# Kernel optimization log

Hardware: AMD Instinct MI355X
Metric: run time of the kernel (lower is better)

The kernel has to match this reference:

```python
import jax, jax.numpy as jnp
import numpy as np

B, C, H_IMG, W_IMG = 16, 384, 56, 56
NUM_HEADS = 6
HEAD_DIM = C // NUM_HEADS
BN_EPS = 1e-5


def _bn(x, gamma, beta, mean, var):
    # x: [b, ch, n] or [b, ch, h, w]; per-channel affine normalization (eval-mode BatchNorm)
    shape = (1, -1) + (1,) * (x.ndim - 2)
    scale = (gamma / jnp.sqrt(var + BN_EPS)).reshape(shape)
    shift = (beta - mean * gamma / jnp.sqrt(var + BN_EPS)).reshape(shape)
    return x * scale + shift


def setup_inputs() -> dict:
    key = jax.random.key(0)
    ks = jax.random.split(key, 12)
    c2 = 2 * C
    return {
        "x": jax.random.normal(ks[0], (B, C, H_IMG, W_IMG), jnp.float32),
        "qk_w": jax.random.normal(ks[1], (c2, C // 2), jnp.float32) * 0.05,
        "qk_gamma": jax.random.uniform(ks[2], (c2,), jnp.float32, 0.5, 1.5),
        "qk_beta": jax.random.normal(ks[3], (c2,), jnp.float32) * 0.1,
        "qk_mean": jax.random.normal(ks[4], (c2,), jnp.float32) * 0.1,
        "qk_var": jax.random.uniform(ks[5], (c2,), jnp.float32, 0.5, 1.5),
        "pe_w": jax.random.normal(ks[6], (C, 1, 3, 3), jnp.float32) * 0.1,
        "pe_gamma": jax.random.uniform(ks[7], (C,), jnp.float32, 0.5, 1.5),
        "pe_beta": jax.random.normal(ks[8], (C,), jnp.float32) * 0.1,
        "pe_mean": jax.random.normal(ks[9], (C,), jnp.float32) * 0.1,
        "pe_var": jax.random.uniform(ks[10], (C,), jnp.float32, 0.5, 1.5),
    }


def reference(x, qk_w, qk_gamma, qk_beta, qk_mean, qk_var,
              pe_w, pe_gamma, pe_beta, pe_mean, pe_var):
    b, c, h, w = x.shape
    n = h * w
    s = n ** (-0.5)
    nh, hd = NUM_HEADS, HEAD_DIM

    # grouped (groups=2) 1x1 conv: out channels [0:c] from input [0:c/2], [c:2c] from [c/2:c]
    xg = x.reshape(b, 2, c // 2, n)                       # [b, 2, c/2, n]
    wg = qk_w.reshape(2, c, c // 2)                       # [group, out_per_group, in_per_group]
    qk = jnp.einsum('bgin,goi->bgon', xg, wg).reshape(b, 2 * c, n)
    qk = _bn(qk, qk_gamma, qk_beta, qk_mean, qk_var)
    qk = jax.nn.elu(qk) + 1.0

    qk = qk.reshape(b, 2, nh, hd, n)
    q, k = qk[:, 0], qk[:, 1]                             # [b, H, d, n]
    v = x.reshape(b, nh, hd, n)                           # [b, H, d, n]

    # kv = (k*s) @ (v^T * s): [b, H, d, d]
    kv = jnp.einsum('bhdn,bhen->bhde', k * s, v * s)
    # numerator: q^T @ kv -> [b, H, n, d]
    num = jnp.einsum('bhdn,bhde->bhne', q, kv)
    # denominator: q^T @ mean_n(k) -> [b, H, n]
    den = jnp.einsum('bhdn,bhd->bhn', q, k.mean(axis=-1)) + 1e-6
    attn = (num / den[..., None]).transpose(0, 1, 3, 2).reshape(b, c, h, w)

    # depthwise 3x3 conv positional encoding on v (= x) + BN
    pe = jax.lax.conv_general_dilated(
        x, pe_w, window_strides=(1, 1), padding=((1, 1), (1, 1)),
        feature_group_count=c, dimension_numbers=('NCHW', 'OIHW', 'NCHW'))
    pe = _bn(pe, pe_gamma, pe_beta, pe_mean, pe_var)

    return attn + pe
```

## Files before the change

### kernel.cpp

```cpp
#include <hip/hip_runtime.h>
#include <math.h>

#define N_SP 3136
#define BN_EPS 1e-5f

typedef __attribute__((ext_vector_type(8))) short short8;
typedef __attribute__((ext_vector_type(4))) float f32x4;

#define K_SZ    (16*384*N_SP)
#define QF_OFF  (K_SZ)
#define QF_FSZ  (16*6*49*8192/2)
#define KVP_OFF (QF_OFF + QF_FSZ)
#define KVP_SZ  (16*6*7*64*80)
#define KVT_OFF (KVP_OFF + KVP_SZ)
#define KVT_FSZ (2*96*80*64/2)
#define WH_OFF  (KVT_OFF + KVT_FSZ)
#define WSPLIT_N (2*384*192)

__device__ __forceinline__ void bsplit(float f, ushort& h, ushort& l) {
    uint u = __float_as_uint(f);
    uint hr = (u + 0x7FFFu + ((u >> 16) & 1u)) >> 16;
    h = (ushort)hr;
    float fh = __uint_as_float(hr << 16);
    float fl = f - fh;
    uint v = __float_as_uint(fl);
    l = (ushort)((v + 0x7FFFu + ((v >> 16) & 1u)) >> 16);
}

__global__ __launch_bounds__(256) void p0_wsplit(
    const float* __restrict__ qk_w, ushort* __restrict__ wh, ushort* __restrict__ wl)
{
    int idx = blockIdx.x * 256 + threadIdx.x;
    if (idx >= WSPLIT_N) return;
    ushort h, l;
    bsplit(qk_w[idx], h, l);
    wh[idx] = h;
    wl[idx] = l;
}

__global__ __launch_bounds__(256) void k1_qk_mfma(
    const float* __restrict__ x, const ushort* __restrict__ wh, const ushort* __restrict__ wl,
    const float* __restrict__ gamma, const float* __restrict__ beta,
    const float* __restrict__ mean, const float* __restrict__ var,
    float* __restrict__ k_out, ushort* __restrict__ qf)
{
    __shared__ __align__(16) ushort Ah[8192];
    __shared__ __align__(16) ushort Al[8192];
    __shared__ __align__(16) ushort Bh[4096];
    __shared__ __align__(16) ushort Bl[4096];

    const int bx = blockIdx.x;
    const int bz = blockIdx.y;
    const int by = blockIdx.z;
    const int b = bz >> 1, gg = bz & 1;
    const int t = threadIdx.x;
    const int lane = t & 63, wv = t >> 6;
    const int wr = wv >> 1, wc = wv & 1;
    const int lg = lane >> 4, l15 = lane & 15;

    f32x4 acc[4][2];
    #pragma unroll
    for (int m = 0; m < 4; ++m)
        #pragma unroll
        for (int nf = 0; nf < 2; ++nf)
            acc[m][nf] = (f32x4){0.f, 0.f, 0.f, 0.f};

    const float* xg = x + (size_t)(b * 384 + gg * 192) * N_SP + bx * 64;
    const ushort* whg = wh + (gg * 384 + by * 128) * 192;
    const ushort* wlg = wl + (gg * 384 + by * 128) * 192;

    for (int kt = 0; kt < 3; ++kt) {
        #pragma unroll
        for (int li = 0; li < 4; ++li) {
            int c = li * 256 + t;
            int row = c >> 3, kb = c & 7;
            int goff = row * 192 + kt * 64 + kb * 8;
            float4 vh = *(const float4*)(whg + goff);
            float4 vl = *(const float4*)(wlg + goff);
            int ch = (row * 8 + (kb ^ (row & 7))) * 8;
            *(float4*)&Ah[ch] = vh;
            *(float4*)&Al[ch] = vl;
        }
        #pragma unroll
        for (int li = 0; li < 2; ++li) {
            int idx = li * 256 + t;
            int kp = idx >> 4;
            int nq = idx & 15;
            int k0 = kp * 2;
            const float* px = xg + (size_t)(kt * 64 + k0) * N_SP + nq * 4;
            float4 v0 = *(const float4*)px;
            float4 v1 = *(const float4*)(px + N_SP);
            ushort h0[4], l0[4], h1[4], l1[4];
            float a0[4] = {v0.x, v0.y, v0.z, v0.w};
            float a1[4] = {v1.x, v1.y, v1.z, v1.w};
            #pragma unroll
            for (int i = 0; i < 4; ++i) { bsplit(a0[i], h0[i], l0[i]); bsplit(a1[i], h1[i], l1[i]); }
            int kb = k0 >> 3, ks = (k0 & 6) >> 1;
            #pragma unroll
            for (int i = 0; i < 4; ++i) {
                int n = nq * 4 + i;
                int chunk = n * 8 + (kb ^ ((n >> 1) & 7));
                ((uint*)Bh)[chunk * 4 + ks] = (uint)h0[i] | ((uint)h1[i] << 16);
                ((uint*)Bl)[chunk * 4 + ks] = (uint)l0[i] | ((uint)l1[i] << 16);
            }
        }
        __syncthreads();
        #pragma unroll
        for (int s = 0; s < 2; ++s) {
            short8 ah[4], al[4], bh[2], bl[2];
            int kb = s * 4 + lg;
            #pragma unroll
            for (int m = 0; m < 4; ++m) {
                int row = wr * 64 + m * 16 + l15;
                int ch = (row * 8 + (kb ^ (row & 7))) * 8;
                ah[m] = *(const short8*)&Ah[ch];
                al[m] = *(const short8*)&Al[ch];
            }
            #pragma unroll
            for (int nf = 0; nf < 2; ++nf) {
                int n = wc * 32 + nf * 16 + l15;
                int ch = (n * 8 + (kb ^ ((n >> 1) & 7))) * 8;
                bh[nf] = *(const short8*)&Bh[ch];
                bl[nf] = *(const short8*)&Bl[ch];
            }
            #pragma unroll
            for (int m = 0; m < 4; ++m)
                #pragma unroll
                for (int nf = 0; nf < 2; ++nf) {
                    acc[m][nf] = __builtin_amdgcn_mfma_f32_16x16x32_bf16(ah[m], bh[nf], acc[m][nf], 0, 0, 0);
                    acc[m][nf] = __builtin_amdgcn_mfma_f32_16x16x32_bf16(ah[m], bl[nf], acc[m][nf], 0, 0, 0);
                    acc[m][nf] = __builtin_amdgcn_mfma_f32_16x16x32_bf16(al[m], bh[nf], acc[m][nf], 0, 0, 0);
                }
        }
        __syncthreads();
    }

    float* scs = (float*)Bh;
    float* shs = scs + 128;
    if (t < 128) {
        int ch = gg * 384 + by * 128 + t;
        float sc = gamma[ch] / sqrtf(var[ch] + BN_EPS);
        scs[t] = sc;
        shs[t] = beta[ch] - mean[ch] * sc;
    }
    __syncthreads();

    if (gg == 0) {
        const int head = by * 2 + wr;
        ushort* qbase = qf + ((size_t)(b * 6 + head) * 49 + bx) * 8192;
        #pragma unroll
        for (int m = 0; m < 4; ++m) {
            #pragma unroll
            for (int nf = 0; nf < 2; ++nf) {
                ushort hh[4], ll[4];
                #pragma unroll
                for (int r = 0; r < 4; ++r) {
                    int orow = wr * 64 + m * 16 + lg * 4 + r;
                    float v = acc[m][nf][r] * scs[orow] + shs[orow];
                    v = v > 0.f ? v + 1.f : __expf(v);
                    bsplit(v, hh[r], ll[r]);
                }
                int hc = m * 4 + lg;
                int n = wc * 32 + nf * 16 + l15;
                uint2 uh, ul;
                uh.x = (uint)hh[0] | ((uint)hh[1] << 16);
                uh.y = (uint)hh[2] | ((uint)hh[3] << 16);
                ul.x = (uint)ll[0] | ((uint)ll[1] << 16);
                ul.y = (uint)ll[2] | ((uint)ll[3] << 16);
                *(uint2*)(qbase + (size_t)hc * 256 + n * 4) = uh;
                *(uint2*)(qbase + (size_t)(16 + hc) * 256 + n * 4) = ul;
            }
        }
    } else {
        size_t obase = ((size_t)b * 384 + by * 128) * N_SP + bx * 64 + wc * 32;
        #pragma unroll
        for (int m = 0; m < 4; ++m)
            #pragma unroll
            for (int nf = 0; nf < 2; ++nf) {
                #pragma unroll
                for (int r = 0; r < 4; ++r) {
                    int orow = wr * 64 + m * 16 + lg * 4 + r;
                    float v = acc[m][nf][r] * scs[orow] + shs[orow];
                    v = v > 0.f ? v + 1.f : __expf(v);
                    k_out[obase + (size_t)orow * N_SP + nf * 16 + l15] = v;
                }
            }
    }
}

__global__ __launch_bounds__(256) void k2_kv_mfma(
    const float* __restrict__ x, const float* __restrict__ kbuf,
    float* __restrict__ kv_part)
{
    __shared__ __align__(16) ushort Kh[4096], Kl[4096];
    __shared__ __align__(16) ushort Vh[5120], Vl[5120];

    const int chunk = blockIdx.x;
    const int h = blockIdx.y, b = blockIdx.z;
    const int t = threadIdx.x;
    const int lane = t & 63, wv = t >> 6;
    const int lg = lane >> 4, l15 = lane & 15;

    const float* kp = kbuf + (size_t)(b*384 + h*64) * N_SP;
    const float* vp = x   + (size_t)(b*384 + h*64) * N_SP;

    #pragma unroll
    for (int li = 0; li < 4; ++li) {
        int idx = li * 256 + t;
        int row = 64 + (idx >> 6), col = idx & 63;
        int off = (row * 8 + ((col >> 3) ^ (row & 7))) * 8 + (col & 7);
        Vh[off] = (row == 64) ? (ushort)0x3F80 : (ushort)0;
        Vl[off] = 0;
    }

    f32x4 acc[5];
    #pragma unroll
    for (int nf = 0; nf < 5; ++nf) acc[nf] = (f32x4){0.f, 0.f, 0.f, 0.f};

    for (int sub = 0; sub < 7; ++sub) {
        int n0 = chunk * 448 + sub * 64;
        #pragma unroll
        for (int li = 0; li < 4; ++li) {
            int idx = li * 256 + t;
            int row = idx >> 4, sc = idx & 15;
            int off = (row * 8 + ((sc >> 1) ^ (row & 7))) * 8 + (sc & 1) * 4;
            float4 kf = *(const float4*)&kp[(size_t)row * N_SP + n0 + sc * 4];
            ushort h0,h1,h2,h3,l0,l1,l2,l3;
            bsplit(kf.x,h0,l0); bsplit(kf.y,h1,l1); bsplit(kf.z,h2,l2); bsplit(kf.w,h3,l3);
            ((uint*)&Kh[off])[0] = (uint)h0 | ((uint)h1 << 16);
            ((uint*)&Kh[off])[1] = (uint)h2 | ((uint)h3 << 16);
            ((uint*)&Kl[off])[0] = (uint)l0 | ((uint)l1 << 16);
            ((uint*)&Kl[off])[1] = (uint)l2 | ((uint)l3 << 16);
            float4 vf = *(const float4*)&vp[(size_t)row * N_SP + n0 + sc * 4];
            bsplit(vf.x,h0,l0); bsplit(vf.y,h1,l1); bsplit(vf.z,h2,l2); bsplit(vf.w,h3,l3);
            ((uint*)&Vh[off])[0] = (uint)h0 | ((uint)h1 << 16);
            ((uint*)&Vh[off])[1] = (uint)h2 | ((uint)h3 << 16);
            ((uint*)&Vl[off])[0] = (uint)l0 | ((uint)l1 << 16);
            ((uint*)&Vl[off])[1] = (uint)l2 | ((uint)l3 << 16);
        }
        __syncthreads();
        #pragma unroll
        for (int s = 0; s < 2; ++s) {
            int arow = wv * 16 + l15;
            int akb = (s * 4 + lg) ^ (arow & 7);
            short8 ah = *(const short8*)&Kh[(arow * 8 + akb) * 8];
            short8 al = *(const short8*)&Kl[(arow * 8 + akb) * 8];
            #pragma unroll
            for (int nf = 0; nf < 5; ++nf) {
                int brow = nf * 16 + l15;
                int bkb = (s * 4 + lg) ^ (brow & 7);
                short8 bh = *(const short8*)&Vh[(brow * 8 + bkb) * 8];
                short8 bl = *(const short8*)&Vl[(brow * 8 + bkb) * 8];
                acc[nf] = __builtin_amdgcn_mfma_f32_16x16x32_bf16(ah, bh, acc[nf], 0, 0, 0);
                acc[nf] = __builtin_amdgcn_mfma_f32_16x16x32_bf16(ah, bl, acc[nf], 0, 0, 0);
                acc[nf] = __builtin_amdgcn_mfma_f32_16x16x32_bf16(al, bh, acc[nf], 0, 0, 0);
            }
        }
        __syncthreads();
    }

    size_t base = (size_t)((b*6 + h)*7 + chunk) * 64 * 80;
    #pragma unroll
    for (int nf = 0; nf < 5; ++nf)
        #pragma unroll
        for (int r = 0; r < 4; ++r) {
            int d = wv * 16 + lg * 4 + r;
            kv_part[base + (size_t)d * 80 + nf * 16 + l15] = acc[nf][r];
        }
}

__global__ __launch_bounds__(256) void k2b_reduce(
    const float* __restrict__ kv_part,
    ushort* __restrict__ kvt_h, ushort* __restrict__ kvt_l)
{
    const int bh = blockIdx.x;
    const int t = threadIdx.x;
    const float inv_n = 1.0f / (float)N_SP;
    const float* base = kv_part + (size_t)bh * 7 * 5120;
    ushort* oh = kvt_h + (size_t)bh * 5120;
    ushort* ol = kvt_l + (size_t)bh * 5120;
    float s[20];
    #pragma unroll
    for (int j = 0; j < 20; ++j) s[j] = 0.f;
    for (int c = 0; c < 7; ++c) {
        #pragma unroll
        for (int j = 0; j < 20; ++j) s[j] += base[c * 5120 + j * 256 + t];
    }
    #pragma unroll
    for (int j = 0; j < 20; ++j) {
        int i = j * 256 + t;
        int d = i / 80, e = i % 80;
        ushort h, l;
        bsplit(s[j] * inv_n, h, l);
        oh[e * 64 + d] = h;
        ol[e * 64 + d] = l;
    }
}

#define ATT_STRIDE 68
__global__ __launch_bounds__(256) void k3_attn_pe(
    const float* __restrict__ x, const ushort* __restrict__ qf,
    const ushort* __restrict__ kvt_h, const ushort* __restrict__ kvt_l,
    const float* __restrict__ pw,
    const float* __restrict__ pgamma, const float* __restrict__ pbeta,
    const float* __restrict__ pmean, const float* __restrict__ pvar,
    float* __restrict__ out)
{
    __shared__ __align__(16) float SBF[ATT_STRIDE * 64 + 64];

    const int bx = blockIdx.x;
    const int h = blockIdx.y, b = blockIdx.z;
    const int t = threadIdx.x;
    const int lane = t & 63, wv = t >> 6;
    const int lg = lane >> 4, l15 = lane & 15;
    const int n0 = bx * 64;

    const ushort* qtile = qf + ((size_t)(b * 6 + h) * 49 + bx) * 8192;
    short8 bqh[2], bql[2];
    #pragma unroll
    for (int s = 0; s < 2; ++s) {
        int hc = (s * 4 + lg) * 2;
        const ushort* ph = qtile + hc * 256 + (wv * 16 + l15) * 4;
        uint2 a0 = *(const uint2*)ph;
        uint2 a1 = *(const uint2*)(ph + 256);
        uint* bh = (uint*)&bqh[s];
        bh[0] = a0.x; bh[1] = a0.y; bh[2] = a1.x; bh[3] = a1.y;
        const ushort* pl = ph + 16 * 256;
        uint2 c0 = *(const uint2*)pl;
        uint2 c1 = *(const uint2*)(pl + 256);
        uint* blp = (uint*)&bql[s];
        blp[0] = c0.x; blp[1] = c0.y; blp[2] = c1.x; blp[3] = c1.y;
    }

    const ushort* ahb = kvt_h + (size_t)(b * 6 + h) * 5120;
    const ushort* alb = kvt_l + (size_t)(b * 6 + h) * 5120;
    f32x4 acc[5];
    #pragma unroll
    for (int m = 0; m < 5; ++m) acc[m] = (f32x4){0.f, 0.f, 0.f, 0.f};
    #pragma unroll
    for (int s = 0; s < 2; ++s) {
        #pragma unroll
        for (int m = 0; m < 5; ++m) {
            int off = (m * 16 + l15) * 64 + (s * 4 + lg) * 8;
            short8 ah = *(const short8*)&ahb[off];
            short8 al = *(const short8*)&alb[off];
            acc[m] = __builtin_amdgcn_mfma_f32_16x16x32_bf16(ah, bqh[s], acc[m], 0, 0, 0);
            acc[m] = __builtin_amdgcn_mfma_f32_16x16x32_bf16(ah, bql[s], acc[m], 0, 0, 0);
            acc[m] = __builtin_amdgcn_mfma_f32_16x16x32_bf16(al, bqh[s], acc[m], 0, 0, 0);
        }
    }

    {
        int ncol = wv * 16 + l15;
        #pragma unroll
        for (int m = 0; m < 4; ++m)
            #pragma unroll
            for (int r = 0; r < 4; ++r)
                SBF[(m * 16 + lg * 4 + r) * ATT_STRIDE + ncol] = acc[m][r];
        if (lg == 0)
            SBF[ATT_STRIDE * 64 + ncol] = acc[4][0];
    }
    __syncthreads();

    const int tx = t & 15, ty = t >> 4;
    const int p0 = n0 + tx * 4;
    const int y = p0 / 56, xc = p0 % 56;
    float den[4];
    #pragma unroll
    for (int p = 0; p < 4; ++p) den[p] = SBF[ATT_STRIDE * 64 + tx * 4 + p] + 1e-6f;
    #pragma unroll
    for (int j = 0; j < 4; ++j) {
        int cc = ty * 4 + j;
        int c = h * 64 + cc;
        const float* xp = x + ((size_t)b * 384 + c) * N_SP;
        float s6[3][6];
        #pragma unroll
        for (int dy = 0; dy < 3; ++dy) {
            int yy = y + dy - 1;
            bool yok = (yy >= 0) && (yy < 56);
            float4 mid = make_float4(0.f, 0.f, 0.f, 0.f);
            float lf = 0.f, rt = 0.f;
            if (yok) {
                const float* xr = xp + yy * 56;
                mid = *(const float4*)&xr[xc];
                if (xc > 0)  lf = xr[xc - 1];
                if (xc < 52) rt = xr[xc + 4];
            }
            s6[dy][0] = lf;  s6[dy][1] = mid.x; s6[dy][2] = mid.y;
            s6[dy][3] = mid.z; s6[dy][4] = mid.w; s6[dy][5] = rt;
        }
        float w9[9];
        #pragma unroll
        for (int q = 0; q < 9; ++q) w9[q] = pw[c * 9 + q];
        float sc2 = pgamma[c] / sqrtf(pvar[c] + BN_EPS);
        float sh2 = pbeta[c] - pmean[c] * sc2;
        float4 r;
        float* pr = (float*)&r;
        #pragma unroll
        for (int p = 0; p < 4; ++p) {
            float conv = 0.f;
            #pragma unroll
            for (int dy = 0; dy < 3; ++dy)
                #pragma unroll
                for (int dx = 0; dx < 3; ++dx)
                    conv += w9[dy * 3 + dx] * s6[dy][p + dx];
            float num = SBF[cc * ATT_STRIDE + tx * 4 + p];
            pr[p] = num / den[p] + (conv * sc2 + sh2);
        }
        *(float4*)&out[((size_t)b * 384 + c) * N_SP + p0] = r;
    }
}

extern "C" void kernel_launch(void* const* d_in, const int* in_sizes, int n_in,
                              void* d_out, int out_size, void* d_ws, size_t ws_size,
                              hipStream_t stream)
{
    const float* x        = (const float*)d_in[0];
    const float* qk_w     = (const float*)d_in[1];
    const float* qk_gamma = (const float*)d_in[2];
    const float* qk_beta  = (const float*)d_in[3];
    const float* qk_mean  = (const float*)d_in[4];
    const float* qk_var   = (const float*)d_in[5];
    const float* pe_w     = (const float*)d_in[6];
    const float* pe_gamma = (const float*)d_in[7];
    const float* pe_beta  = (const float*)d_in[8];
    const float* pe_mean  = (const float*)d_in[9];
    const float* pe_var   = (const float*)d_in[10];
    float* out = (float*)d_out;

    float* ws      = (float*)d_ws;
    float* kbuf    = ws;
    ushort* qf     = (ushort*)(ws + QF_OFF);
    float* kv_part = ws + KVP_OFF;
    ushort* kvt_h  = (ushort*)(ws + KVT_OFF);
    ushort* kvt_l  = kvt_h + 96 * 5120;
    ushort* whp    = (ushort*)(ws + WH_OFF);
    ushort* wlp    = whp + WSPLIT_N;

    hipLaunchKernelGGL(p0_wsplit, dim3((WSPLIT_N + 255)/256), dim3(256), 0, stream,
                       qk_w, whp, wlp);
    dim3 g1(49, 32, 3);
    hipLaunchKernelGGL(k1_qk_mfma, g1, dim3(256), 0, stream,
                       x, whp, wlp, qk_gamma, qk_beta, qk_mean, qk_var, kbuf, qf);
    dim3 g2(7, 6, 16);
    hipLaunchKernelGGL(k2_kv_mfma, g2, dim3(256), 0, stream, x, kbuf, kv_part);
    hipLaunchKernelGGL(k2b_reduce, dim3(96), dim3(256), 0, stream,
                       kv_part, kvt_h, kvt_l);
    dim3 g3(49, 6, 16);
    hipLaunchKernelGGL(k3_attn_pe, g3, dim3(256), 0, stream,
                       x, qf, kvt_h, kvt_l, pe_w, pe_gamma, pe_beta, pe_mean, pe_var, out);
}
```

Baseline: 225.4 us.

## Process seven spatial tiles per block with KV staged in swizzled LDS

After: 222.2 us. About the same (-1.4%).

```diff
diff --git a/kernel.cpp b/kernel.cpp
--- a/kernel.cpp
+++ b/kernel.cpp
@@ -297,6 +297,25 @@
     }
 }
 
+__device__ __forceinline__ void load_qfrag(const ushort* qtile, int wv, int lg, int l15,
+                                           short8* qh, short8* ql)
+{
+    #pragma unroll
+    for (int s = 0; s < 2; ++s) {
+        int hc = (s * 4 + lg) * 2;
+        const ushort* ph = qtile + hc * 256 + (wv * 16 + l15) * 4;
+        uint2 a0 = *(const uint2*)ph;
+        uint2 a1 = *(const uint2*)(ph + 256);
+        uint* bh = (uint*)&qh[s];
+        bh[0] = a0.x; bh[1] = a0.y; bh[2] = a1.x; bh[3] = a1.y;
+        const ushort* pl = ph + 16 * 256;
+        uint2 c0 = *(const uint2*)pl;
+        uint2 c1 = *(const uint2*)(pl + 256);
+        uint* bl = (uint*)&ql[s];
+        bl[0] = c0.x; bl[1] = c0.y; bl[2] = c1.x; bl[3] = c1.y;
+    }
+}
+
 #define ATT_STRIDE 68
 __global__ __launch_bounds__(256) void k3_attn_pe(
     const float* __restrict__ x, const ushort* __restrict__ qf,
@@ -306,108 +325,121 @@
     const float* __restrict__ pmean, const float* __restrict__ pvar,
     float* __restrict__ out)
 {
+    __shared__ __align__(16) ushort KVH[5120], KVL[5120];
     __shared__ __align__(16) float SBF[ATT_STRIDE * 64 + 64];
 
-    const int bx = blockIdx.x;
     const int h = blockIdx.y, b = blockIdx.z;
     const int t = threadIdx.x;
     const int lane = t & 63, wv = t >> 6;
     const int lg = lane >> 4, l15 = lane & 15;
-    const int n0 = bx * 64;
-
-    const ushort* qtile = qf + ((size_t)(b * 6 + h) * 49 + bx) * 8192;
-    short8 bqh[2], bql[2];
-    #pragma unroll
-    for (int s = 0; s < 2; ++s) {
-        int hc = (s * 4 + lg) * 2;
-        const ushort* ph = qtile + hc * 256 + (wv * 16 + l15) * 4;
-        uint2 a0 = *(const uint2*)ph;
-        uint2 a1 = *(const uint2*)(ph + 256);
-        uint* bh = (uint*)&bqh[s];
-        bh[0] = a0.x; bh[1] = a0.y; bh[2] = a1.x; bh[3] = a1.y;
-        const ushort* pl = ph + 16 * 256;
-        uint2 c0 = *(const uint2*)pl;
-        uint2 c1 = *(const uint2*)(pl + 256);
-        uint* blp = (uint*)&bql[s];
-        blp[0] = c0.x; blp[1] = c0.y; blp[2] = c1.x; blp[3] = c1.y;
-    }
-
-    const ushort* ahb = kvt_h + (size_t)(b * 6 + h) * 5120;
-    const ushort* alb = kvt_l + (size_t)(b * 6 + h) * 5120;
-    f32x4 acc[5];
-    #pragma unroll
-    for (int m = 0; m < 5; ++m) acc[m] = (f32x4){0.f, 0.f, 0.f, 0.f};
-    #pragma unroll
-    for (int s = 0; s < 2; ++s) {
-        #pragma unroll
-        for (int m = 0; m < 5; ++m) {
-            int off = (m * 16 + l15) * 64 + (s * 4 + lg) * 8;
-            short8 ah = *(const short8*)&ahb[off];
-            short8 al = *(const short8*)&alb[off];
-            acc[m] = __builtin_amdgcn_mfma_f32_16x16x32_bf16(ah, bqh[s], acc[m], 0, 0, 0);
-            acc[m] = __builtin_amdgcn_mfma_f32_16x16x32_bf16(ah, bql[s], acc[m], 0, 0, 0);
-            acc[m] = __builtin_amdgcn_mfma_f32_16x16x32_bf16(al, bqh[s], acc[m], 0, 0, 0);
-        }
-    }
-
-    {
-        int ncol = wv * 16 + l15;
-        #pragma unroll
-        for (int m = 0; m < 4; ++m)
-            #pragma unroll
-            for (int r = 0; r < 4; ++r)
-                SBF[(m * 16 + lg * 4 + r) * ATT_STRIDE + ncol] = acc[m][r];
-        if (lg == 0)
-            SBF[ATT_STRIDE * 64 + ncol] = acc[4][0];
-    }
+
+    const ushort* gh = kvt_h + (size_t)(b * 6 + h) * 5120;
+    const ushort* gl = kvt_l + (size_t)(b * 6 + h) * 5120;
+    for (int c = t; c < 640; c += 256) {
+        int e = c >> 3, i = c & 7;
+        int dst = (e * 8 + (i ^ (e & 7))) * 8;
+        *(float4*)&KVH[dst] = *(const float4*)&gh[c * 8];
+        *(float4*)&KVL[dst] = *(const float4*)&gl[c * 8];
+    }
+
+    const ushort* qstrip = qf + ((size_t)(b * 6 + h) * 49 + blockIdx.x * 7) * 8192;
+    short8 qch[2], qcl[2], qnh[2], qnl[2];
+    load_qfrag(qstrip, wv, lg, l15, qch, qcl);
     __syncthreads();
 
     const int tx = t & 15, ty = t >> 4;
-    const int p0 = n0 + tx * 4;
-    const int y = p0 / 56, xc = p0 % 56;
-    float den[4];
-    #pragma unroll
-    for (int p = 0; p < 4; ++p) den[p] = SBF[ATT_STRIDE * 64 + tx * 4 + p] + 1e-6f;
+    float sc2[4], sh2[4], w9[4][9];
     #pragma unroll
     for (int j = 0; j < 4; ++j) {
-        int cc = ty * 4 + j;
-        int c = h * 64 + cc;
-        const float* xp = x + ((size_t)b * 384 + c) * N_SP;
-        float s6[3][6];
-        #pragma unroll
-        for (int dy = 0; dy < 3; ++dy) {
-            int yy = y + dy - 1;
-            bool yok = (yy >= 0) && (yy < 56);
-            float4 mid = make_float4(0.f, 0.f, 0.f, 0.f);
-            float lf = 0.f, rt = 0.f;
-            if (yok) {
-                const float* xr = xp + yy * 56;
-                mid = *(const float4*)&xr[xc];
-                if (xc > 0)  lf = xr[xc - 1];
-                if (xc < 52) rt = xr[xc + 4];
-            }
-            s6[dy][0] = lf;  s6[dy][1] = mid.x; s6[dy][2] = mid.y;
-            s6[dy][3] = mid.z; s6[dy][4] = mid.w; s6[dy][5] = rt;
-        }
-        float w9[9];
-        #pragma unroll
-        for (int q = 0; q < 9; ++q) w9[q] = pw[c * 9 + q];
-        float sc2 = pgamma[c] / sqrtf(pvar[c] + BN_EPS);
-        float sh2 = pbeta[c] - pmean[c] * sc2;
-        float4 r;
-        float* pr = (float*)&r;
-        #pragma unroll
-        for (int p = 0; p < 4; ++p) {
-            float conv = 0.f;
-            #pragma unroll
-            for (int dy = 0; dy < 3; ++dy)
+        int c = h * 64 + ty * 4 + j;
+        sc2[j] = pgamma[c] / sqrtf(pvar[c] + BN_EPS);
+        sh2[j] = pbeta[c] - pmean[c] * sc2[j];
+        #pragma unroll
+        for (int q = 0; q < 9; ++q) w9[j][q] = pw[c * 9 + q];
+    }
+
+    for (int tt = 0; tt < 7; ++tt) {
+        const int bx = blockIdx.x * 7 + tt;
+        const int n0 = bx * 64;
+
+        if (tt < 6)
+            load_qfrag(qstrip + (size_t)(tt + 1) * 8192, wv, lg, l15, qnh, qnl);
+
+        f32x4 acc[5];
+        #pragma unroll
+        for (int m = 0; m < 5; ++m) acc[m] = (f32x4){0.f, 0.f, 0.f, 0.f};
+        #pragma unroll
+        for (int s = 0; s < 2; ++s) {
+            #pragma unroll
+            for (int m = 0; m < 5; ++m) {
+                int off = ((m * 16 + l15) * 8 + ((s * 4 + lg) ^ (l15 & 7))) * 8;
+                short8 ah = *(const short8*)&KVH[off];
+                short8 al = *(const short8*)&KVL[off];
+                acc[m] = __builtin_amdgcn_mfma_f32_16x16x32_bf16(ah, qch[s], acc[m], 0, 0, 0);
+                acc[m] = __builtin_amdgcn_mfma_f32_16x16x32_bf16(ah, qcl[s], acc[m], 0, 0, 0);
+                acc[m] = __builtin_amdgcn_mfma_f32_16x16x32_bf16(al, qch[s], acc[m], 0, 0, 0);
+            }
+        }
+
+        {
+            int ncol = wv * 16 + l15;
+            #pragma unroll
+            for (int m = 0; m < 4; ++m)
                 #pragma unroll
-                for (int dx = 0; dx < 3; ++dx)
-                    conv += w9[dy * 3 + dx] * s6[dy][p + dx];
-            float num = SBF[cc * ATT_STRIDE + tx * 4 + p];
-            pr[p] = num / den[p] + (conv * sc2 + sh2);
-        }
-        *(float4*)&out[((size_t)b * 384 + c) * N_SP + p0] = r;
+                for (int r = 0; r < 4; ++r)
+                    SBF[(m * 16 + lg * 4 + r) * ATT_STRIDE + ncol] = acc[m][r];
+            if (lg == 0)
+                SBF[ATT_STRIDE * 64 + ncol] = acc[4][0];
+        }
+        __syncthreads();
+
+        const int p0 = n0 + tx * 4;
+        const int y = p0 / 56, xc = p0 % 56;
+        float den[4];
+        #pragma unroll
+        for (int p = 0; p < 4; ++p) den[p] = SBF[ATT_STRIDE * 64 + tx * 4 + p] + 1e-6f;
+        #pragma unroll
+        for (int j = 0; j < 4; ++j) {
+            int cc = ty * 4 + j;
+            int c = h * 64 + cc;
+            const float* xp = x + ((size_t)b * 384 + c) * N_SP;
+            float s6[3][6];
+            #pragma unroll
+            for (int dy = 0; dy < 3; ++dy) {
+                int yy = y + dy - 1;
+                bool yok = (yy >= 0) && (yy < 56);
+                float4 mid = make_float4(0.f, 0.f, 0.f, 0.f);
+                float lf = 0.f, rt = 0.f;
+                if (yok) {
+                    const float* xr = xp + yy * 56;
+                    mid = *(const float4*)&xr[xc];
+                    if (xc > 0)  lf = xr[xc - 1];
+                    if (xc < 52) rt = xr[xc + 4];
+                }
+                s6[dy][0] = lf;  s6[dy][1] = mid.x; s6[dy][2] = mid.y;
+                s6[dy][3] = mid.z; s6[dy][4] = mid.w; s6[dy][5] = rt;
+            }
+            float4 r;
+            float* pr = (float*)&r;
+            #pragma unroll
+            for (int p = 0; p < 4; ++p) {
+                float conv = 0.f;
+                #pragma unroll
+                for (int dy = 0; dy < 3; ++dy)
+                    #pragma unroll
+                    for (int dx = 0; dx < 3; ++dx)
+                        conv += w9[j][dy * 3 + dx] * s6[dy][p + dx];
+                float num = SBF[cc * ATT_STRIDE + tx * 4 + p];
+                pr[p] = num / den[p] + (conv * sc2[j] + sh2[j]);
+            }
+            *(float4*)&out[((size_t)b * 384 + c) * N_SP + p0] = r;
+        }
+
+        if (tt < 6) {
+            __syncthreads();
+            #pragma unroll
+            for (int s = 0; s < 2; ++s) { qch[s] = qnh[s]; qcl[s] = qnl[s]; }
+        }
     }
 }
 
@@ -446,7 +478,7 @@
     hipLaunchKernelGGL(k2_kv_mfma, g2, dim3(256), 0, stream, x, kbuf, kv_part);
     hipLaunchKernelGGL(k2b_reduce, dim3(96), dim3(256), 0, stream,
                        kv_part, kvt_h, kvt_l);
-    dim3 g3(49, 6, 16);
+    dim3 g3(7, 6, 16);
     hipLaunchKernelGGL(k3_attn_pe, g3, dim3(256), 0, stream,
                        x, qf, kvt_h, kvt_l, pe_w, pe_gamma, pe_beta, pe_mean, pe_var, out);
 }
```

## Split fused attention+PE kernel into separate attention and depthwise-conv kernels

Applied to the files above, without the earlier changes.

Measured after the change: 238.8 us. 1.06x slower.

```diff
diff --git a/kernel.cpp b/kernel.cpp
--- a/kernel.cpp
+++ b/kernel.cpp
@@ -297,13 +297,29 @@
     }
 }
 
+__device__ __forceinline__ void load_qfrag(const ushort* qtile, int wv, int lg, int l15,
+                                           short8* qh, short8* ql)
+{
+    #pragma unroll
+    for (int s = 0; s < 2; ++s) {
+        int hc = (s * 4 + lg) * 2;
+        const ushort* ph = qtile + hc * 256 + (wv * 16 + l15) * 4;
+        uint2 a0 = *(const uint2*)ph;
+        uint2 a1 = *(const uint2*)(ph + 256);
+        uint* bh = (uint*)&qh[s];
+        bh[0] = a0.x; bh[1] = a0.y; bh[2] = a1.x; bh[3] = a1.y;
+        const ushort* pl = ph + 16 * 256;
+        uint2 c0 = *(const uint2*)pl;
+        uint2 c1 = *(const uint2*)(pl + 256);
+        uint* bl = (uint*)&ql[s];
+        bl[0] = c0.x; bl[1] = c0.y; bl[2] = c1.x; bl[3] = c1.y;
+    }
+}
+
 #define ATT_STRIDE 68
-__global__ __launch_bounds__(256) void k3_attn_pe(
-    const float* __restrict__ x, const ushort* __restrict__ qf,
+__global__ __launch_bounds__(256) void k3a_attn(
+    const ushort* __restrict__ qf,
     const ushort* __restrict__ kvt_h, const ushort* __restrict__ kvt_l,
-    const float* __restrict__ pw,
-    const float* __restrict__ pgamma, const float* __restrict__ pbeta,
-    const float* __restrict__ pmean, const float* __restrict__ pvar,
     float* __restrict__ out)
 {
     __shared__ __align__(16) float SBF[ATT_STRIDE * 64 + 64];
@@ -317,20 +333,7 @@
 
     const ushort* qtile = qf + ((size_t)(b * 6 + h) * 49 + bx) * 8192;
     short8 bqh[2], bql[2];
-    #pragma unroll
-    for (int s = 0; s < 2; ++s) {
-        int hc = (s * 4 + lg) * 2;
-        const ushort* ph = qtile + hc * 256 + (wv * 16 + l15) * 4;
-        uint2 a0 = *(const uint2*)ph;
-        uint2 a1 = *(const uint2*)(ph + 256);
-        uint* bh = (uint*)&bqh[s];
-        bh[0] = a0.x; bh[1] = a0.y; bh[2] = a1.x; bh[3] = a1.y;
-        const ushort* pl = ph + 16 * 256;
-        uint2 c0 = *(const uint2*)pl;
-        uint2 c1 = *(const uint2*)(pl + 256);
-        uint* blp = (uint*)&bql[s];
-        blp[0] = c0.x; blp[1] = c0.y; blp[2] = c1.x; blp[3] = c1.y;
-    }
+    load_qfrag(qtile, wv, lg, l15, bqh, bql);
 
     const ushort* ahb = kvt_h + (size_t)(b * 6 + h) * 5120;
     const ushort* alb = kvt_l + (size_t)(b * 6 + h) * 5120;
@@ -364,7 +367,6 @@
 
     const int tx = t & 15, ty = t >> 4;
     const int p0 = n0 + tx * 4;
-    const int y = p0 / 56, xc = p0 % 56;
     float den[4];
     #pragma unroll
     for (int p = 0; p < 4; ++p) den[p] = SBF[ATT_STRIDE * 64 + tx * 4 + p] + 1e-6f;
@@ -372,42 +374,71 @@
     for (int j = 0; j < 4; ++j) {
         int cc = ty * 4 + j;
         int c = h * 64 + cc;
-        const float* xp = x + ((size_t)b * 384 + c) * N_SP;
-        float s6[3][6];
+        float4 r;
+        float* pr = (float*)&r;
+        #pragma unroll
+        for (int p = 0; p < 4; ++p)
+            pr[p] = SBF[cc * ATT_STRIDE + tx * 4 + p] / den[p];
+        *(float4*)&out[((size_t)b * 384 + c) * N_SP + p0] = r;
+    }
+}
+
+__global__ __launch_bounds__(256) void k3b_pe(
+    const float* __restrict__ x, const float* __restrict__ pw,
+    const float* __restrict__ pgamma, const float* __restrict__ pbeta,
+    const float* __restrict__ pmean, const float* __restrict__ pvar,
+    float* __restrict__ out)
+{
+    const int bc = blockIdx.x;
+    const int c = bc & 383;
+    const int cc = bc % 384;
+    (void)c;
+    const float* xp = x + (size_t)bc * N_SP;
+    float* op = out + (size_t)bc * N_SP;
+    float w9[9];
+    #pragma unroll
+    for (int q = 0; q < 9; ++q) w9[q] = pw[cc * 9 + q];
+    float sc = pgamma[cc] / sqrtf(pvar[cc] + BN_EPS);
+    float sh = pbeta[cc] - pmean[cc] * sc;
+
+    for (int s = threadIdx.x; s < 392; s += 256) {
+        int y = s / 7, xs = (s % 7) * 8;
+        float row[3][10];
         #pragma unroll
         for (int dy = 0; dy < 3; ++dy) {
             int yy = y + dy - 1;
             bool yok = (yy >= 0) && (yy < 56);
-            float4 mid = make_float4(0.f, 0.f, 0.f, 0.f);
-            float lf = 0.f, rt = 0.f;
             if (yok) {
                 const float* xr = xp + yy * 56;
-                mid = *(const float4*)&xr[xc];
-                if (xc > 0)  lf = xr[xc - 1];
-                if (xc < 52) rt = xr[xc + 4];
-            }
-            s6[dy][0] = lf;  s6[dy][1] = mid.x; s6[dy][2] = mid.y;
-            s6[dy][3] = mid.z; s6[dy][4] = mid.w; s6[dy][5] = rt;
-        }
-        float w9[9];
-        #pragma unroll
-        for (int q = 0; q < 9; ++q) w9[q] = pw[c * 9 + q];
-        float sc2 = pgamma[c] / sqrtf(pvar[c] + BN_EPS);
-        float sh2 = pbeta[c] - pmean[c] * sc2;
-        float4 r;
-        float* pr = (float*)&r;
-        #pragma unroll
-        for (int p = 0; p < 4; ++p) {
+                float4 a = *(const float4*)&xr[xs];
+                float4 bq = *(const float4*)&xr[xs + 4];
+                row[dy][1] = a.x;  row[dy][2] = a.y;  row[dy][3] = a.z;  row[dy][4] = a.w;
+                row[dy][5] = bq.x; row[dy][6] = bq.y; row[dy][7] = bq.z; row[dy][8] = bq.w;
+                row[dy][0] = (xs > 0)  ? xr[xs - 1] : 0.f;
+                row[dy][9] = (xs < 48) ? xr[xs + 8] : 0.f;
+            } else {
+                #pragma unroll
+                for (int i = 0; i < 10; ++i) row[dy][i] = 0.f;
+            }
+        }
+        float* po = op + y * 56 + xs;
+        float4 o0 = *(const float4*)po;
+        float4 o1 = *(const float4*)(po + 4);
+        float ov[8] = {o0.x, o0.y, o0.z, o0.w, o1.x, o1.y, o1.z, o1.w};
+        #pragma unroll
+        for (int p = 0; p < 8; ++p) {
             float conv = 0.f;
             #pragma unroll
             for (int dy = 0; dy < 3; ++dy)
                 #pragma unroll
                 for (int dx = 0; dx < 3; ++dx)
-                    conv += w9[dy * 3 + dx] * s6[dy][p + dx];
-            float num = SBF[cc * ATT_STRIDE + tx * 4 + p];
-            pr[p] = num / den[p] + (conv * sc2 + sh2);
-        }
-        *(float4*)&out[((size_t)b * 384 + c) * N_SP + p0] = r;
+                    conv += w9[dy * 3 + dx] * row[dy][p + dx];
+            ov[p] += conv * sc + sh;
+        }
+        float4 r0 = make_float4(ov[0], ov[1], ov[2], ov[3]);
+        float4 r1 = make_float4(ov[4], ov[5], ov[6], ov[7]);
+        *(float4*)po = r0;
+        *(float4*)(po + 4) = r1;
     }
 }
 
@@ -447,6 +478,8 @@
     hipLaunchKernelGGL(k2b_reduce, dim3(96), dim3(256), 0, stream,
                        kv_part, kvt_h, kvt_l);
     dim3 g3(49, 6, 16);
-    hipLaunchKernelGGL(k3_attn_pe, g3, dim3(256), 0, stream,
-                       x, qf, kvt_h, kvt_l, pe_w, pe_gamma, pe_beta, pe_mean, pe_var, out);
-}
+    hipLaunchKernelGGL(k3a_attn, g3, dim3(256), 0, stream,
+                       qf, kvt_h, kvt_l, out);
+    hipLaunchKernelGGL(k3b_pe, dim3(6144), dim3(256), 0, stream,
+                       x, pe_w, pe_gamma, pe_beta, pe_mean, pe_var, out);
+}
```
